# Kernel optimization log

Hardware: AMD Instinct MI355X
Metric: run time of the kernel (lower is better)

Reference implementation:

```python
import jax, jax.numpy as jnp
import numpy as np

NUM_USERS = 100000
NUM_ITEMS = 50000
N_NODES = NUM_USERS + NUM_ITEMS
NUM_COMMUNITY = 64
N_LAYERS = 3
NNZ = 2400000
BATCH = 8192
NEG_SLOPE = 0.1
EPS = 1e-12


def setup_inputs() -> dict:
    key = jax.random.key(0)
    ks = jax.random.split(key, 9)
    stdv = 1.0 / np.sqrt(NUM_COMMUNITY)
    return {
        "users": jax.random.randint(ks[0], (BATCH,), 0, NUM_USERS, dtype=jnp.int64 if jax.config.jax_enable_x64 else jnp.int32).astype(jnp.int32),
        "adjacent_items": jax.random.randint(ks[1], (BATCH,), 0, NUM_ITEMS).astype(jnp.int32),
        "weak_items": jax.random.randint(ks[2], (BATCH,), 0, NUM_ITEMS).astype(jnp.int32),
        "strong_items": jax.random.randint(ks[3], (BATCH,), 0, NUM_ITEMS).astype(jnp.int32),
        "edge_rows": jax.random.randint(ks[4], (NNZ,), 0, N_NODES).astype(jnp.int32),
        "edge_cols": jax.random.randint(ks[5], (NNZ,), 0, N_NODES).astype(jnp.int32),
        "edge_vals": jax.random.uniform(ks[6], (NNZ,), dtype=jnp.float32),
        "user_preference": jax.random.uniform(ks[7], (NUM_USERS, NUM_COMMUNITY), dtype=jnp.float32, minval=-stdv, maxval=stdv),
        "item_preference": jax.random.uniform(ks[8], (NUM_ITEMS, NUM_COMMUNITY), dtype=jnp.float32, minval=-stdv, maxval=stdv),
    }


def _lrelu_l2norm(x):
    # leaky_relu(neg_slope=0.1) then L2-normalize along last dim (torch F.normalize semantics)
    x = jnp.where(x >= 0, x, NEG_SLOPE * x)
    norm = jnp.sqrt(jnp.sum(x * x, axis=-1, keepdims=True))
    return x / jnp.maximum(norm, EPS)


def reference(users, adjacent_items, weak_items, strong_items,
              edge_rows, edge_cols, edge_vals,
              user_preference, item_preference):
    # ---- computer(): LightGCN-style propagation over sparse adjacency ----
    pref = _lrelu_l2norm(jnp.concatenate([user_preference, item_preference], axis=0))  # [N, C]
    acc = pref
    p = pref
    for _ in range(N_LAYERS):
        # sparse.mm(Graph, p): gather source rows, scale by edge values, scatter-add into dest rows
        msg = edge_vals[:, None] * p[edge_cols]                      # [nnz, C]
        p = jax.ops.segment_sum(msg, edge_rows, num_segments=N_NODES)  # [N, C]
        p = _lrelu_l2norm(p)
        acc = acc + p
    merged = acc / (N_LAYERS + 1)  # mean over stacked layers
    users_pref = merged[:NUM_USERS]
    items_pref = merged[NUM_USERS:]

    # ---- forward(): per-pair dot products + sigmoid ----
    u = users_pref[users]  # [B, C]

    def score(items):
        return jax.nn.sigmoid(jnp.sum(u * items_pref[items], axis=-1))

    # stack of (adjacent, weak, strong) gamma preferences, shape [3, B]
    return jnp.stack([score(adjacent_items), score(weak_items), score(strong_items)], axis=0)
```

## Files before the change

kernel.cpp:

```cpp
#include <hip/hip_runtime.h>
#include <hip/hip_fp16.h>
#include <math.h>

#define D 64
#define NUM_USERS 100000
#define NUM_ITEMS 50000
#define N_NODES 150000
#define NNZ 2400000
#define BATCH 8192
#define NEG_SLOPE 0.1f
#define EPS_NRM 1e-12f

#define NB2     293
#define RPB     512
#define NCHUNK  256
#define CH      9376
#define CAPB    9472
#define HCAP    4736
#define CAPH    5120
#define VSCALE  16383.f

typedef unsigned short ushort_t;
typedef int   iv4 __attribute__((ext_vector_type(4)));
typedef float fv4 __attribute__((ext_vector_type(4)));

__device__ __forceinline__ float wave_sum64(float v) {
    #pragma unroll
    for (int off = 32; off > 0; off >>= 1)
        v += __shfl_xor(v, off, 64);
    return v;
}

__device__ __forceinline__ float h2f_lo(unsigned u) {
    return __half2float(__ushort_as_half((unsigned short)(u & 0xFFFFu)));
}
__device__ __forceinline__ float h2f_hi(unsigned u) {
    return __half2float(__ushort_as_half((unsigned short)(u >> 16)));
}

__global__ void __launch_bounds__(1024) scatter_init(
        const int* __restrict__ rows, const int* __restrict__ cols,
        const float* __restrict__ vals, int* __restrict__ gcur,
        uint2* __restrict__ es8,
        const float* __restrict__ upref, const float* __restrict__ ipref,
        __half* __restrict__ p0) {
    __shared__ int cnt[NB2];
    __shared__ int cur[NB2];
    int blk = blockIdx.x, tid = threadIdx.x;

    if (blk >= NCHUNK) {
        int row  = (blk - NCHUNK) * 16 + (tid >> 6);
        int lane = tid & 63;
        if (row >= N_NODES) return;
        float x = (row < NUM_USERS) ? upref[(size_t)row * D + lane]
                                    : ipref[(size_t)(row - NUM_USERS) * D + lane];
        x = (x >= 0.f) ? x : NEG_SLOPE * x;
        float norm = sqrtf(wave_sum64(x * x));
        float y = x / fmaxf(norm, EPS_NRM);
        p0[(size_t)row * D + lane] = __float2half(y);
        return;
    }

    for (int b = tid; b < NB2; b += 1024) cnt[b] = 0;
    __syncthreads();
    int base = blk * CH;
    int n = NNZ - base; if (n > CH) n = CH;
    const iv4* r4 = (const iv4*)(rows + base);
    for (int i = tid; i < (n >> 2); i += 1024) {
        iv4 r = r4[i];
        atomicAdd(&cnt[r.x >> 9], 1);
        atomicAdd(&cnt[r.y >> 9], 1);
        atomicAdd(&cnt[r.z >> 9], 1);
        atomicAdd(&cnt[r.w >> 9], 1);
    }
    __syncthreads();
    if (tid < NB2) {
        int c = cnt[tid];
        int off = (c > 0) ? atomicAdd(&gcur[tid], c) : 0;
        cur[tid] = tid * CAPB + off;
    }
    __syncthreads();
    const iv4* c4 = (const iv4*)(cols + base);
    const fv4* v4 = (const fv4*)(vals + base);
    for (int i = tid; i < (n >> 2); i += 1024) {
        iv4 r  = r4[i];
        iv4 cc = __builtin_nontemporal_load(&c4[i]);
        fv4 v  = __builtin_nontemporal_load(&v4[i]);
        int p;
        p = atomicAdd(&cur[r.x >> 9], 1);
        es8[p] = make_uint2((unsigned)cc.x | ((unsigned)(v.x * VSCALE + 0.5f) << 18),
                            (unsigned)(r.x & (RPB - 1)));
        p = atomicAdd(&cur[r.y >> 9], 1);
        es8[p] = make_uint2((unsigned)cc.y | ((unsigned)(v.y * VSCALE + 0.5f) << 18),
                            (unsigned)(r.y & (RPB - 1)));
        p = atomicAdd(&cur[r.z >> 9], 1);
        es8[p] = make_uint2((unsigned)cc.z | ((unsigned)(v.z * VSCALE + 0.5f) << 18),
                            (unsigned)(r.z & (RPB - 1)));
        p = atomicAdd(&cur[r.w >> 9], 1);
        es8[p] = make_uint2((unsigned)cc.w | ((unsigned)(v.w * VSCALE + 0.5f) << 18),
                            (unsigned)(r.w & (RPB - 1)));
    }
}

__global__ void __launch_bounds__(512) bucket_sort(const uint2* __restrict__ es8,
                                                   const int* __restrict__ gcur,
                                                   unsigned* __restrict__ es,
                                                   int2* __restrict__ rowptr2) {
    __shared__ int      hist[256];
    __shared__ int      wsum[4];
    __shared__ unsigned outbuf[CAPH];
    __shared__ int      sh_total;
    int blk = blockIdx.x, tid = threadIdx.x;
    int b = blk >> 1, h = blk & 1;
    int base = b * CAPB;
    int fill = gcur[b];
    int end  = base + fill;
    int obase = base + h * HCAP;
    if (tid < 256) hist[tid] = 0;
    __syncthreads();
    for (int i = base + tid; i < end; i += 512) {
        unsigned k = es8[i].y;
        if ((int)(k >> 8) == h) atomicAdd(&hist[k & 255], 1);
    }
    __syncthreads();
    int excl = 0, v = 0;
    if (tid < 256) {
        v = hist[tid];
        int lane = tid & 63, w = tid >> 6;
        int s = v;
        #pragma unroll
        for (int off = 1; off < 64; off <<= 1) {
            int t = __shfl_up(s, off, 64);
            if (lane >= off) s += t;
        }
        if (lane == 63) wsum[w] = s;
        excl = s - v;
    }
    __syncthreads();
    if (tid == 0) {
        int a = 0;
        #pragma unroll
        for (int i = 0; i < 4; i++) { int t = wsum[i]; wsum[i] = a; a += t; }
    }
    __syncthreads();
    if (tid < 256) {
        excl += wsum[tid >> 6];
        int r = b * RPB + h * 256 + tid;
        if (r < N_NODES)
            rowptr2[r] = make_int2(obase + excl, obase + excl + v);
        if (tid == 255) sh_total = excl + v;
        hist[tid] = excl;
    }
    __syncthreads();
    for (int i = base + tid; i < end; i += 512) {
        uint2 kv = es8[i];
        if ((int)(kv.y >> 8) == h) {
            int d = atomicAdd(&hist[kv.y & 255], 1);
            outbuf[d] = kv.x;
        }
    }
    __syncthreads();
    int total = sh_total;
    for (int i = tid; i < total; i += 512)
        es[obase + i] = outbuf[i];
}

__device__ __forceinline__ void acc8(float a[8], float v, uint4 q) {
    a[0] = fmaf(v, h2f_lo(q.x), a[0]);
    a[1] = fmaf(v, h2f_hi(q.x), a[1]);
    a[2] = fmaf(v, h2f_lo(q.y), a[2]);
    a[3] = fmaf(v, h2f_hi(q.y), a[3]);
    a[4] = fmaf(v, h2f_lo(q.z), a[4]);
    a[5] = fmaf(v, h2f_hi(q.z), a[5]);
    a[6] = fmaf(v, h2f_lo(q.w), a[6]);
    a[7] = fmaf(v, h2f_hi(q.w), a[7]);
}

__global__ void gather_kernel(const int2* __restrict__ rowptr2,
                              const unsigned* __restrict__ es,
                              const __half* __restrict__ p,
                              __half* __restrict__ pn) {
    int tid  = threadIdx.x;
    int row  = blockIdx.x * 8 + (tid >> 5);
    if (row >= N_NODES) return;
    int hl   = tid & 31;
    int sub  = hl >> 3;
    int fl   = hl & 7;
    int2 rp  = rowptr2[row];
    int beg = rp.x, end = rp.y;

    float a[8];
    #pragma unroll
    for (int k = 0; k < 8; k++) a[k] = 0.f;

    const float vs = 1.f / VSCALE;
    int e = beg + sub;
    while (e + 4 < end) {
        unsigned ev0 = es[e];
        unsigned ev1 = es[e + 4];
        const uint4 q0 = *(const uint4*)(p + (((ev0 & 0x3FFFFu) << 6) | (fl << 3)));
        const uint4 q1 = *(const uint4*)(p + (((ev1 & 0x3FFFFu) << 6) | (fl << 3)));
        float v0 = (float)(ev0 >> 18) * vs;
        float v1 = (float)(ev1 >> 18) * vs;
        acc8(a, v0, q0);
        acc8(a, v1, q1);
        e += 8;
    }
    if (e < end) {
        unsigned ev = es[e];
        const uint4 q = *(const uint4*)(p + (((ev & 0x3FFFFu) << 6) | (fl << 3)));
        float v = (float)(ev >> 18) * vs;
        acc8(a, v, q);
    }

    bool s0 = (sub & 1) != 0, s1 = (sub & 2) != 0;
    float b1[4];
    #pragma unroll
    for (int j = 0; j < 4; j++) {
        int c4 = (j >> 1) * 4, bb = j & 1;
        float keep = s0 ? a[c4 + 2 + bb] : a[c4 + bb];
        float send = s0 ? a[c4 + bb]     : a[c4 + 2 + bb];
        b1[j] = keep + __shfl_xor(send, 8, 64);
    }
    float cf[2];
    #pragma unroll
    for (int bb = 0; bb < 2; bb++) {
        float keep = s1 ? b1[2 + bb] : b1[bb];
        float send = s1 ? b1[bb]     : b1[2 + bb];
        cf[bb] = keep + __shfl_xor(send, 16, 64);
    }
    float y0 = (cf[0] >= 0.f) ? cf[0] : NEG_SLOPE * cf[0];
    float y1 = (cf[1] >= 0.f) ? cf[1] : NEG_SLOPE * cf[1];
    float ss = fmaf(y0, y0, y1 * y1);
    ss += __shfl_xor(ss, 16, 64);
    ss += __shfl_xor(ss, 8, 64);
    ss += __shfl_xor(ss, 4, 64);
    ss += __shfl_xor(ss, 2, 64);
    ss += __shfl_xor(ss, 1, 64);
    float inv = 1.f / fmaxf(sqrtf(ss), EPS_NRM);
    __half2 o = __floats2half2_rn(y0 * inv, y1 * inv);
    *(__half2*)(pn + (size_t)row * D + fl * 8 + 2 * sub) = o;
}

__global__ void score_kernel(const int* __restrict__ users,
                             const int* __restrict__ it0,
                             const int* __restrict__ it1,
                             const int* __restrict__ it2,
                             const __half* __restrict__ p0,
                             const __half* __restrict__ p1,
                             const __half* __restrict__ p2,
                             const __half* __restrict__ p3,
                             float* __restrict__ out) {
    int b    = blockIdx.x * 4 + (threadIdx.x >> 6);
    int lane = threadIdx.x & 63;
    if (b >= BATCH) return;
    int u = users[b];
    size_t uo = (size_t)u * D + lane;
    float uf = __half2float(p0[uo]) + __half2float(p1[uo])
             + __half2float(p2[uo]) + __half2float(p3[uo]);

    int its[3];
    its[0] = it0[b]; its[1] = it1[b]; its[2] = it2[b];
    #pragma unroll
    for (int k = 0; k < 3; k++) {
        size_t io = (size_t)(NUM_USERS + its[k]) * D + lane;
        float itf = __half2float(p0[io]) + __half2float(p1[io])
                  + __half2float(p2[io]) + __half2float(p3[io]);
        float s = wave_sum64(uf * itf) * 0.0625f;
        if (lane == 0)
            out[k * BATCH + b] = 1.f / (1.f + expf(-s));
    }
}

extern "C" void kernel_launch(void* const* d_in, const int* in_sizes, int n_in,
                              void* d_out, int out_size, void* d_ws, size_t ws_size,
                              hipStream_t stream) {
    const int*   users  = (const int*)  d_in[0];
    const int*   adj    = (const int*)  d_in[1];
    const int*   weak   = (const int*)  d_in[2];
    const int*   strong = (const int*)  d_in[3];
    const int*   erows  = (const int*)  d_in[4];
    const int*   ecols  = (const int*)  d_in[5];
    const float* evals  = (const float*)d_in[6];
    const float* upref  = (const float*)d_in[7];
    const float* ipref  = (const float*)d_in[8];
    float* out = (float*)d_out;

    const size_t rowElems = (size_t)N_NODES * D;

    char* base = (char*)d_ws;
    size_t off = 0;
    auto alloc = [&](size_t bytes) {
        char* p = base + off;
        off = (off + bytes + 255) & ~(size_t)255;
        return (void*)p;
    };
    __half*   p0      = (__half*)  alloc(rowElems * sizeof(__half));
    __half*   p1      = (__half*)  alloc(rowElems * sizeof(__half));
    __half*   p2      = (__half*)  alloc(rowElems * sizeof(__half));
    __half*   p3      = (__half*)  alloc(rowElems * sizeof(__half));
    unsigned* es      = (unsigned*)alloc((size_t)NB2 * CAPB * 4);
    int2*     rowptr2 = (int2*)    alloc((size_t)N_NODES * sizeof(int2));
    int*      gcur    = (int*)     alloc(NB2 * sizeof(int));
    uint2*    es8t    = (uint2*)p2;

    hipMemsetAsync(gcur, 0, NB2 * sizeof(int), stream);
    scatter_init<<<NCHUNK + (N_NODES + 15) / 16, 1024, 0, stream>>>(
        erows, ecols, evals, gcur, es8t, upref, ipref, p0);
    bucket_sort<<<NB2 * 2, 512, 0, stream>>>(es8t, gcur, es, rowptr2);

    gather_kernel<<<N_NODES / 8, 256, 0, stream>>>(rowptr2, es, p0, p1);
    gather_kernel<<<N_NODES / 8, 256, 0, stream>>>(rowptr2, es, p1, p2);
    gather_kernel<<<N_NODES / 8, 256, 0, stream>>>(rowptr2, es, p2, p3);

    score_kernel<<<(BATCH + 3) / 4, 256, 0, stream>>>(users, adj, weak, strong,
                                                      p0, p1, p2, p3, out);
}
```

Baseline: 327.0 us.

## Fuse bucket sort with first propagation layer gather, reading edges from LDS

Merges the bucket-sort kernel with the first gather layer: each sort block keeps its sorted edge slice in shared memory and computes the layer-1 aggregation, leaky-ReLU and L2 normalization for its 256 rows straight from LDS. This removes one kernel launch and the global re-read of the sorted edge list for layer 1. It also shrinks the LDS output buffer and adds a 4-way unrolled loop to the remaining gather kernels for more loads in flight. In exchange, the first layer now runs on only 586 blocks instead of many small ones, which may lower parallelism and latency hiding. The smaller buffer also risks overflow if a bucket half holds more edges than it fits.

```diff
diff --git a/kernel.cpp b/kernel.cpp
--- a/kernel.cpp
+++ b/kernel.cpp
@@ -17,7 +17,7 @@
 #define CH      9376
 #define CAPB    9472
 #define HCAP    4736
-#define CAPH    5120
+#define CAPH    4864
 #define VSCALE  16383.f
 
 typedef unsigned short ushort_t;
@@ -36,6 +36,17 @@
 }
 __device__ __forceinline__ float h2f_hi(unsigned u) {
     return __half2float(__ushort_as_half((unsigned short)(u >> 16)));
+}
+
+__device__ __forceinline__ void acc8(float a[8], float v, uint4 q) {
+    a[0] = fmaf(v, h2f_lo(q.x), a[0]);
+    a[1] = fmaf(v, h2f_hi(q.x), a[1]);
+    a[2] = fmaf(v, h2f_lo(q.y), a[2]);
+    a[3] = fmaf(v, h2f_hi(q.y), a[3]);
+    a[4] = fmaf(v, h2f_lo(q.z), a[4]);
+    a[5] = fmaf(v, h2f_hi(q.z), a[5]);
+    a[6] = fmaf(v, h2f_lo(q.w), a[6]);
+    a[7] = fmaf(v, h2f_hi(q.w), a[7]);
 }
 
 __global__ void __launch_bounds__(1024) scatter_init(
@@ -102,14 +113,14 @@
     }
 }
 
-__global__ void __launch_bounds__(512) bucket_sort(const uint2* __restrict__ es8,
-                                                   const int* __restrict__ gcur,
-                                                   unsigned* __restrict__ es,
-                                                   int2* __restrict__ rowptr2) {
+__global__ void __launch_bounds__(512) sort_gather1(
+        const uint2* __restrict__ es8, const int* __restrict__ gcur,
+        unsigned* __restrict__ es, int2* __restrict__ rowptr2,
+        const __half* __restrict__ p0, __half* __restrict__ p1) {
     __shared__ int      hist[256];
+    __shared__ int      rbeg[256];
     __shared__ int      wsum[4];
     __shared__ unsigned outbuf[CAPH];
-    __shared__ int      sh_total;
     int blk = blockIdx.x, tid = threadIdx.x;
     int b = blk >> 1, h = blk & 1;
     int base = b * CAPB;
@@ -118,6 +129,7 @@
     int obase = base + h * HCAP;
     if (tid < 256) hist[tid] = 0;
     __syncthreads();
+
     for (int i = base + tid; i < end; i += 512) {
         unsigned k = es8[i].y;
         if ((int)(k >> 8) == h) atomicAdd(&hist[k & 255], 1);
@@ -148,7 +160,7 @@
         int r = b * RPB + h * 256 + tid;
         if (r < N_NODES)
             rowptr2[r] = make_int2(obase + excl, obase + excl + v);
-        if (tid == 255) sh_total = excl + v;
+        rbeg[tid] = excl;
         hist[tid] = excl;
     }
     __syncthreads();
@@ -160,20 +172,71 @@
         }
     }
     __syncthreads();
-    int total = sh_total;
+    int total = hist[255];
     for (int i = tid; i < total; i += 512)
         es[obase + i] = outbuf[i];
-}
-
-__device__ __forceinline__ void acc8(float a[8], float v, uint4 q) {
-    a[0] = fmaf(v, h2f_lo(q.x), a[0]);
-    a[1] = fmaf(v, h2f_hi(q.x), a[1]);
-    a[2] = fmaf(v, h2f_lo(q.y), a[2]);
-    a[3] = fmaf(v, h2f_hi(q.y), a[3]);
-    a[4] = fmaf(v, h2f_lo(q.z), a[4]);
-    a[5] = fmaf(v, h2f_hi(q.z), a[5]);
-    a[6] = fmaf(v, h2f_lo(q.w), a[6]);
-    a[7] = fmaf(v, h2f_hi(q.w), a[7]);
+
+    int hl  = tid & 31;
+    int sub = hl >> 3;
+    int fl  = hl & 7;
+    const float vs = 1.f / VSCALE;
+    for (int pass = 0; pass < 16; pass++) {
+        int lr  = pass * 16 + (tid >> 5);
+        int row = b * RPB + h * 256 + lr;
+        if (row >= N_NODES) continue;
+        int lbeg = rbeg[lr], lend = hist[lr];
+
+        float a[8];
+        #pragma unroll
+        for (int k = 0; k < 8; k++) a[k] = 0.f;
+
+        int e = lbeg + sub;
+        while (e + 4 < lend) {
+            unsigned ev0 = outbuf[e];
+            unsigned ev1 = outbuf[e + 4];
+            const uint4 q0 = *(const uint4*)(p0 + (((ev0 & 0x3FFFFu) << 6) | (fl << 3)));
+            const uint4 q1 = *(const uint4*)(p0 + (((ev1 & 0x3FFFFu) << 6) | (fl << 3)));
+            float v0 = (float)(ev0 >> 18) * vs;
+            float v1 = (float)(ev1 >> 18) * vs;
+            acc8(a, v0, q0);
+            acc8(a, v1, q1);
+            e += 8;
+        }
+        if (e < lend) {
+            unsigned ev = outbuf[e];
+            const uint4 q = *(const uint4*)(p0 + (((ev & 0x3FFFFu) << 6) | (fl << 3)));
+            float v = (float)(ev >> 18) * vs;
+            acc8(a, v, q);
+        }
+
+        bool s0 = (sub & 1) != 0, s1 = (sub & 2) != 0;
+        float b1[4];
+        #pragma unroll
+        for (int j = 0; j < 4; j++) {
+            int c4 = (j >> 1) * 4, bb = j & 1;
+            float keep = s0 ? a[c4 + 2 + bb] : a[c4 + bb];
+            float send = s0 ? a[c4 + bb]     : a[c4 + 2 + bb];
+            b1[j] = keep + __shfl_xor(send, 8, 64);
+        }
+        float cf[2];
+        #pragma unroll
+        for (int bb = 0; bb < 2; bb++) {
+            float keep = s1 ? b1[2 + bb] : b1[bb];
+            float send = s1 ? b1[bb]     : b1[2 + bb];
+            cf[bb] = keep + __shfl_xor(send, 16, 64);
+        }
+        float y0 = (cf[0] >= 0.f) ? cf[0] : NEG_SLOPE * cf[0];
+        float y1 = (cf[1] >= 0.f) ? cf[1] : NEG_SLOPE * cf[1];
+        float ss = fmaf(y0, y0, y1 * y1);
+        ss += __shfl_xor(ss, 16, 64);
+        ss += __shfl_xor(ss, 8, 64);
+        ss += __shfl_xor(ss, 4, 64);
+        ss += __shfl_xor(ss, 2, 64);
+        ss += __shfl_xor(ss, 1, 64);
+        float inv = 1.f / fmaxf(sqrtf(ss), EPS_NRM);
+        __half2 o = __floats2half2_rn(y0 * inv, y1 * inv);
+        *(__half2*)(p1 + (size_t)row * D + fl * 8 + 2 * sub) = o;
+    }
 }
 
 __global__ void gather_kernel(const int2* __restrict__ rowptr2,
@@ -195,6 +258,25 @@
 
     const float vs = 1.f / VSCALE;
     int e = beg + sub;
+    while (e + 12 < end) {
+        unsigned ev0 = es[e];
+        unsigned ev1 = es[e + 4];
+        unsigned ev2 = es[e + 8];
+        unsigned ev3 = es[e + 12];
+        const uint4 q0 = *(const uint4*)(p + (((ev0 & 0x3FFFFu) << 6) | (fl << 3)));
+        const uint4 q1 = *(const uint4*)(p + (((ev1 & 0x3FFFFu) << 6) | (fl << 3)));
+        const uint4 q2 = *(const uint4*)(p + (((ev2 & 0x3FFFFu) << 6) | (fl << 3)));
+        const uint4 q3 = *(const uint4*)(p + (((ev3 & 0x3FFFFu) << 6) | (fl << 3)));
+        float v0 = (float)(ev0 >> 18) * vs;
+        float v1 = (float)(ev1 >> 18) * vs;
+        float v2 = (float)(ev2 >> 18) * vs;
+        float v3 = (float)(ev3 >> 18) * vs;
+        acc8(a, v0, q0);
+        acc8(a, v1, q1);
+        acc8(a, v2, q2);
+        acc8(a, v3, q3);
+        e += 16;
+    }
     while (e + 4 < end) {
         unsigned ev0 = es[e];
         unsigned ev1 = es[e + 4];
@@ -307,9 +389,8 @@
     hipMemsetAsync(gcur, 0, NB2 * sizeof(int), stream);
     scatter_init<<<NCHUNK + (N_NODES + 15) / 16, 1024, 0, stream>>>(
         erows, ecols, evals, gcur, es8t, upref, ipref, p0);
-    bucket_sort<<<NB2 * 2, 512, 0, stream>>>(es8t, gcur, es, rowptr2);
-
-    gather_kernel<<<N_NODES / 8, 256, 0, stream>>>(rowptr2, es, p0, p1);
+    sort_gather1<<<NB2 * 2, 512, 0, stream>>>(es8t, gcur, es, rowptr2, p0, p1);
+
     gather_kernel<<<N_NODES / 8, 256, 0, stream>>>(rowptr2, es, p1, p2);
     gather_kernel<<<N_NODES / 8, 256, 0, stream>>>(rowptr2, es, p2, p3);
 
```

After: 331.9 us. No clear change (+1.5%).
